# Performance work log

Measured on AMD Instinct MI355X. Metric: run time of the kernel, lower is better.

The kernel has to match this reference:

```python
import jax, jax.numpy as jnp
import numpy as np

# e2m1 nibble -> float LUT (indices 0..7 positive, 8..15 negative), per mxfp4 spec
E2M1_LUT = jnp.array([0.0, 0.5, 1.0, 1.5, 2.0, 3.0, 4.0, 6.0,
                      -0.0, -0.5, -1.0, -1.5, -2.0, -3.0, -4.0, -6.0], dtype=jnp.float32)


def mxfp4_dequant(scales, blocks):
    """scales: [E, R, K//32] int (uint8 values); blocks: [E, R, K//32, 16] int (uint8 values).
    Returns dequantized weight [E, K, R] (transposed like the original)."""
    low = blocks & 15
    high = (blocks >> 4) & 15
    interleaved = jnp.stack([low, high], axis=-1)            # [E, R, K//32, 16, 2]
    interleaved = interleaved.reshape(blocks.shape[:-1] + (32,))  # [E, R, K//32, 32]
    vals = E2M1_LUT[interleaved]                             # [E, R, K//32, 32] f32
    exp = scales.astype(jnp.int32) - 127                     # biased uint8 exponent
    deq = jnp.ldexp(vals, exp[..., None])                    # scale each block
    deq = deq.reshape(deq.shape[:-2] + (-1,))                # [E, R, K]
    return deq.transpose(0, 2, 1)                            # [E, K, R]


def rmsnorm(x, w, eps=1e-5):
    var = jnp.mean(x * x, axis=-1, keepdims=True)
    return x * jax.lax.rsqrt(var + eps) * w


def setup_inputs() -> dict:
    key = jax.random.key(0)
    ks = jax.random.split(key, 8)
    T, H, D, E = 1024, 2048, 2048, 8
    return {
        "x": jax.random.normal(ks[0], (T, H), dtype=jnp.float32),
        "norm_weight": jnp.ones((H,), dtype=jnp.float32),
        "router_weight": jax.random.normal(ks[1], (H, E), dtype=jnp.float32) * 0.02,
        "router_bias": jnp.zeros((E,), dtype=jnp.float32),
        "gate_up_scales": jax.random.randint(ks[2], (E, 2 * D, H // 32), 0, 132, dtype=jnp.int32),
        "gate_up_blocks": jax.random.randint(ks[3], (E, 2 * D, H // 32, 16), 0, 256, dtype=jnp.int32),
        "gate_up_bias": jax.random.normal(ks[4], (E, 2 * D), dtype=jnp.float32) * 0.02,
        "down_scales": jax.random.randint(ks[5], (E, H, D // 32), 0, 132, dtype=jnp.int32),
        "down_blocks": jax.random.randint(ks[6], (E, H, D // 32, 16), 0, 256, dtype=jnp.int32),
        "down_bias": jax.random.normal(ks[7], (E, H), dtype=jnp.float32) * 0.02,
        "k": 4,
    }


def reference(x, norm_weight, router_weight, router_bias,
              gate_up_scales, gate_up_blocks, gate_up_bias,
              down_scales, down_blocks, down_bias, k):
    alpha, limit = 1.702, 7.0
    W_gu = mxfp4_dequant(gate_up_scales, gate_up_blocks)   # [E, H, 2D]
    W_down = mxfp4_dequant(down_scales, down_blocks)       # [E, D, H]

    t = rmsnorm(x, norm_weight)                            # [T, H]
    logits = t @ router_weight + router_bias               # [T, E]
    top_v, top_i = jax.lax.top_k(logits, k)                # [T, k]
    top_v = jax.nn.softmax(top_v, axis=-1)
    tok = jnp.arange(logits.shape[0])[:, None]             # [T, 1]
    scores = jnp.zeros_like(logits).at[tok, top_i].set(top_v)  # [T, E]

    # dense all-expert compute, masked post-hoc by router scores (as in original)
    gate_up = jnp.einsum('th,ehd->etd', t, W_gu) + gate_up_bias[:, None, :]  # [E, T, 2D]
    gate = jnp.minimum(gate_up[..., ::2], limit)
    up = jnp.clip(gate_up[..., 1::2], -limit, limit)
    glu = gate * jax.nn.sigmoid(gate * alpha)
    nxt = jnp.einsum('etd,edh->eth', (up + 1.0) * glu, W_down) + down_bias[:, None, :]  # [E, T, H]
    nxt = nxt * scores.T[..., None]                        # weight by router scores
    return jnp.sum(nxt, axis=0) + x
```

## Files before the change

### kernel.cpp

```cpp
#include <hip/hip_runtime.h>
#include <hip/hip_bf16.h>
#include <stdint.h>

#define T_TOK 1024
#define HDIM 2048
#define DDIM 2048
#define NE 8

typedef unsigned int uint;
typedef unsigned short ushort;

typedef _Float16 f16x8 __attribute__((ext_vector_type(8)));
typedef float f32x4 __attribute__((ext_vector_type(4)));

typedef __attribute__((address_space(1))) const void v_g;
typedef __attribute__((address_space(3))) void v_l;

__device__ __forceinline__ ushort f2h(float f) {
  _Float16 h = (_Float16)f;
  return *(ushort*)&h;
}

__device__ __forceinline__ uint dqh(uint nib, int sc) {
  uint m = nib & 7u;
  int e = (int)(m >> 1);
  int e16 = sc - 113 + e;
  uint mant = ((m & 1u) && m >= 2u) ? 0x200u : 0u;
  uint bits;
  if (m == 0u || e16 <= -10) bits = 0u;
  else if (e16 >= 1) bits = ((uint)e16 << 10) | mant;
  else bits = (0x400u | mant) >> (1 - e16);
  return bits | ((nib & 8u) << 12);
}
__device__ __forceinline__ uint dq2h(uint b, int sc) {
  return dqh(b & 15u, sc) | (dqh((b >> 4) & 15u, sc) << 16);
}

__device__ __forceinline__ void waitv4() {
  asm volatile("s_waitcnt vmcnt(4)" ::: "memory");
  __builtin_amdgcn_sched_barrier(0);
}
__device__ __forceinline__ void waitv0() {
  asm volatile("s_waitcnt vmcnt(0)" ::: "memory");
  __builtin_amdgcn_sched_barrier(0);
}
__device__ __forceinline__ void barrier_raw() {
  asm volatile("" ::: "memory");
  __builtin_amdgcn_s_barrier();
  asm volatile("" ::: "memory");
}

__device__ __forceinline__ void router_body(
    int t, const float* __restrict__ x, const float* __restrict__ nw,
    const float* __restrict__ rw, const float* __restrict__ rb,
    ushort* __restrict__ tbuf, float* __restrict__ scores)
{
  const int tid = threadIdx.x;
  const float4* xr = (const float4*)(x + (size_t)t * HDIM);
  float4 v0 = xr[tid * 2], v1 = xr[tid * 2 + 1];
  float ss = v0.x*v0.x + v0.y*v0.y + v0.z*v0.z + v0.w*v0.w
           + v1.x*v1.x + v1.y*v1.y + v1.z*v1.z + v1.w*v1.w;
  __shared__ float red[256];
  red[tid] = ss;
  __syncthreads();
  for (int s = 128; s > 0; s >>= 1) {
    if (tid < s) red[tid] += red[tid + s];
    __syncthreads();
  }
  const float rstd = rsqrtf(red[0] * (1.0f / HDIM) + 1e-5f);
  float xv[8] = {v0.x, v0.y, v0.z, v0.w, v1.x, v1.y, v1.z, v1.w};
  float lp[NE];
#pragma unroll
  for (int e = 0; e < NE; ++e) lp[e] = 0.f;
  union { ushort us[8]; uint4 v; } pkh;
  const int h0 = tid * 8;
#pragma unroll
  for (int j = 0; j < 8; ++j) {
    int h = h0 + j;
    float tn = xv[j] * rstd * nw[h];
    pkh.us[j] = f2h(tn);
#pragma unroll
    for (int e = 0; e < NE; ++e) lp[e] += tn * rw[h * NE + e];
  }
  *(uint4*)(tbuf + (size_t)t * HDIM + h0) = pkh.v;
#pragma unroll
  for (int e = 0; e < NE; ++e)
#pragma unroll
    for (int off = 32; off > 0; off >>= 1) lp[e] += __shfl_down(lp[e], off);
  __shared__ float wred[4][NE];
  if ((tid & 63) == 0) {
#pragma unroll
    for (int e = 0; e < NE; ++e) wred[tid >> 6][e] = lp[e];
  }
  __syncthreads();
  if (tid == 0) {
    float lg[NE];
#pragma unroll
    for (int e = 0; e < NE; ++e)
      lg[e] = wred[0][e] + wred[1][e] + wred[2][e] + wred[3][e] + rb[e];
    bool used[NE] = {false, false, false, false, false, false, false, false};
    float tv[4]; int ti[4];
    for (int s = 0; s < 4; ++s) {
      float best = -3.4e38f; int bi = 0;
      for (int e = 0; e < NE; ++e)
        if (!used[e] && lg[e] > best) { best = lg[e]; bi = e; }
      used[bi] = true; tv[s] = best; ti[s] = bi;
    }
    float den = 0.f, ev[4];
    for (int s = 0; s < 4; ++s) { ev[s] = expf(tv[s] - tv[0]); den += ev[s]; }
    float so[NE] = {0, 0, 0, 0, 0, 0, 0, 0};
    for (int s = 0; s < 4; ++s) so[ti[s]] = ev[s] / den;
#pragma unroll
    for (int e = 0; e < NE; ++e) scores[t * NE + e] = so[e];
  }
}

__global__ __launch_bounds__(256) void router_kernel(
    const float* __restrict__ x, const float* __restrict__ nw,
    const float* __restrict__ rw, const float* __restrict__ rb,
    ushort* __restrict__ tbuf, float* __restrict__ scores)
{
  router_body(blockIdx.x, x, nw, rw, rb, tbuf, scores);
}

#define NDQB ((NE * 4096 * 64 + NE * 2048 * 64) / 256)
__global__ __launch_bounds__(256) void prep_kernel(
    const float* __restrict__ x, const float* __restrict__ nw,
    const float* __restrict__ rw, const float* __restrict__ rb,
    const int* __restrict__ gub, const int* __restrict__ gus,
    const int* __restrict__ dnb, const int* __restrict__ dns,
    ushort* __restrict__ tbuf, float* __restrict__ scores,
    ushort* __restrict__ wgu, ushort* __restrict__ wdn)
{
  if (blockIdx.x >= NDQB) {
    router_body(blockIdx.x - NDQB, x, nw, rw, rb, tbuf, scores);
    return;
  }
  const int NG = NE * 4096 * 64;
  int tidg = blockIdx.x * 256 + threadIdx.x;
  const int* qb; const int* qs; ushort* dst; int bi;
  if (tidg < NG) { bi = tidg; qb = gub; qs = gus; dst = wgu; }
  else           { bi = tidg - NG; qb = dnb; qs = dns; dst = wdn; }
  int sc = qs[bi];
  const int4* bp = (const int4*)(qb + (size_t)bi * 16);
  int4 q0 = bp[0], q1 = bp[1], q2 = bp[2], q3 = bp[3];
  uint w[16];
  w[0]=dq2h(q0.x,sc);  w[1]=dq2h(q0.y,sc);  w[2]=dq2h(q0.z,sc);  w[3]=dq2h(q0.w,sc);
  w[4]=dq2h(q1.x,sc);  w[5]=dq2h(q1.y,sc);  w[6]=dq2h(q1.z,sc);  w[7]=dq2h(q1.w,sc);
  w[8]=dq2h(q2.x,sc);  w[9]=dq2h(q2.y,sc);  w[10]=dq2h(q2.z,sc); w[11]=dq2h(q2.w,sc);
  w[12]=dq2h(q3.x,sc); w[13]=dq2h(q3.y,sc); w[14]=dq2h(q3.z,sc); w[15]=dq2h(q3.w,sc);
  uint4* o = (uint4*)(dst + (size_t)bi * 32);
  o[0] = make_uint4(w[0], w[1], w[2], w[3]);
  o[1] = make_uint4(w[4], w[5], w[6], w[7]);
  o[2] = make_uint4(w[8], w[9], w[10], w[11]);
  o[3] = make_uint4(w[12], w[13], w[14], w[15]);
}

__global__ __launch_bounds__(256) void scan_kernel(
    const float* __restrict__ scores, int* __restrict__ cnts, int* __restrict__ idx)
{
  const int e = blockIdx.x, tid = threadIdx.x;
  int loc[4], c = 0;
#pragma unroll
  for (int j = 0; j < 4; ++j) {
    int t = tid * 4 + j;
    loc[j] = (scores[t * NE + e] != 0.f) ? 1 : 0;
    c += loc[j];
  }
  __shared__ int sc[256];
  sc[tid] = c;
  __syncthreads();
  for (int off = 1; off < 256; off <<= 1) {
    int v = (tid >= off) ? sc[tid - off] : 0;
    __syncthreads();
    sc[tid] += v;
    __syncthreads();
  }
  int base = sc[tid] - c;
#pragma unroll
  for (int j = 0; j < 4; ++j)
    if (loc[j]) idx[e * T_TOK + base++] = tid * 4 + j;
  if (tid == 255) cnts[e] = sc[255];
}

template<int MODE>
__global__ __launch_bounds__(256) void mx_gemm_p(
    const ushort* __restrict__ Abase,
    const ushort* __restrict__ Bw,
    const float* __restrict__ bias,
    const float* __restrict__ scores,
    const int* __restrict__ cnts,
    const int* __restrict__ tokidx,
    ushort* __restrict__ midH,
    float* __restrict__ outp)
{
  constexpr int NTOT = (MODE == 0) ? 2 * DDIM : HDIM;
  constexpr int K    = (MODE == 0) ? HDIM : DDIM;
  constexpr int NKT  = K / 32;
  const int nt = blockIdx.x, mt = blockIdx.y, e = blockIdx.z;
  const int cnt = cnts[e];
  const int m0 = mt * 128, n0 = nt * 128;
  if (m0 >= cnt) return;
  const ushort* A = Abase + (MODE == 0 ? (size_t)0 : (size_t)e * T_TOK * DDIM);

  __shared__ __align__(16) ushort As[2][128 * 32];
  __shared__ __align__(16) ushort Bs[2][128 * 32];
  __shared__ int tok_s[128];

  const int tid = threadIdx.x;
  const int lane = tid & 63;
  const int wv = tid >> 6;
  const int wm = wv >> 1, wn = wv & 1;
  const int fr = lane & 15, kg = lane >> 4;

  if (tid < 128) {
    int sl = m0 + tid;
    tok_s[tid] = (sl < cnt) ? tokidx[e * T_TOK + sl] : 0;
  }
  __syncthreads();

  int arow[2];
#pragma unroll
  for (int j = 0; j < 2; ++j) {
    int row = (tid + 256 * j) >> 2;
    arow[j] = (MODE == 0) ? tok_s[row] : (m0 + row);
  }

  f32x4 acc[4][4];
#pragma unroll
  for (int i = 0; i < 4; ++i)
#pragma unroll
    for (int j = 0; j < 4; ++j) acc[i][j] = f32x4{0.f, 0.f, 0.f, 0.f};

  auto do_stage = [&](int buf, int kt) {
#pragma unroll
    for (int j = 0; j < 2; ++j) {
      int cidx = tid + 256 * j;
      int row = cidx >> 2, ck = cidx & 3;
      int gck = ck ^ ((row >> 1) & 3);
      size_t go = (size_t)arow[j] * K + kt * 32 + gck * 8;
      __builtin_amdgcn_global_load_lds((v_g*)(A + go),
          (v_l*)((char*)&As[buf][0] + cidx * 16), 16, 0, 0);
    }
#pragma unroll
    for (int j = 0; j < 2; ++j) {
      int cidx = tid + 256 * j;
      int row = cidx >> 2, ck = cidx & 3;
      int gck = ck ^ ((row >> 1) & 3);
      const ushort* g = Bw + ((size_t)e * NTOT + n0 + row) * K + kt * 32 + gck * 8;
      __builtin_amdgcn_global_load_lds((v_g*)g,
          (v_l*)((char*)&Bs[buf][0] + cidx * 16), 16, 0, 0);
    }
  };

  auto do_compute = [&](int buf) {
    f16x8 aF[4], bF[4];
#pragma unroll
    for (int mi = 0; mi < 4; ++mi) {
      int r = wm * 64 + mi * 16 + fr;
      int ck = kg ^ ((r >> 1) & 3);
      aF[mi] = *(const f16x8*)(&As[buf][r * 32 + ck * 8]);
    }
#pragma unroll
    for (int ni = 0; ni < 4; ++ni) {
      int r = wn * 64 + ni * 16 + fr;
      int ck = kg ^ ((r >> 1) & 3);
      bF[ni] = *(const f16x8*)(&Bs[buf][r * 32 + ck * 8]);
    }
#pragma unroll
    for (int mi = 0; mi < 4; ++mi)
#pragma unroll
      for (int ni = 0; ni < 4; ++ni)
        acc[mi][ni] = __builtin_amdgcn_mfma_f32_16x16x32_f16(aF[mi], bF[ni], acc[mi][ni], 0, 0, 0);
  };

  do_stage(0, 0);
  do_stage(1, 1);
  waitv4();
  barrier_raw();
#pragma unroll 2
  for (int kt = 0; kt < NKT; ++kt) {
    do_compute(kt & 1);
    if (kt == NKT - 1) break;
    barrier_raw();
    if (kt + 2 < NKT) {
      do_stage(kt & 1, kt + 2);
      waitv4();
    } else {
      waitv0();
    }
    barrier_raw();
  }

  const int c = lane & 15, rg = lane >> 4;
  const int sbase = m0 + wm * 64, nbase = n0 + wn * 64;
  if constexpr (MODE == 0) {
#pragma unroll
    for (int mi = 0; mi < 4; ++mi)
#pragma unroll
      for (int ni = 0; ni < 4; ++ni) {
        int n = nbase + ni * 16 + c;
        float bv = bias[(size_t)e * NTOT + n];
#pragma unroll
        for (int r = 0; r < 4; ++r) {
          int slot = sbase + mi * 16 + rg * 4 + r;
          float val = acc[mi][ni][r] + bv;
          float other = __shfl_xor(val, 1);
          if (!(c & 1) && slot < cnt) {
            int tok = tok_s[slot - m0];
            float g = fminf(val, 7.0f);
            float u = fminf(fmaxf(other, -7.0f), 7.0f);
            float glu = g / (1.0f + expf(-1.702f * g));
            float mv = (u + 1.0f) * glu;
            float s = scores[tok * NE + e];
            midH[((size_t)e * T_TOK + slot) * DDIM + ((uint)n >> 1)] = f2h(mv * s);
          }
        }
      }
  } else {
#pragma unroll
    for (int mi = 0; mi < 4; ++mi)
#pragma unroll
      for (int ni = 0; ni < 4; ++ni) {
        int n = nbase + ni * 16 + c;
        float dbv = bias[(size_t)e * NTOT + n];
#pragma unroll
        for (int r = 0; r < 4; ++r) {
          int slot = sbase + mi * 16 + rg * 4 + r;
          if (slot < cnt) {
            int tok = tok_s[slot - m0];
            float s = scores[tok * NE + e];
            atomicAdd(outp + (size_t)tok * HDIM + n, acc[mi][ni][r] + s * dbv);
          }
        }
      }
  }
}

__global__ __launch_bounds__(256) void gu_gemm_q(
    const ushort* __restrict__ At,
    const int* __restrict__ qblocks,
    const int* __restrict__ qscales,
    const float* __restrict__ bias,
    const float* __restrict__ scores,
    const int* __restrict__ cnts,
    const int* __restrict__ tokidx,
    ushort* __restrict__ midH)
{
  constexpr int NTOT = 2 * DDIM;
  constexpr int K = HDIM;
  const int nt = blockIdx.x, mt = blockIdx.y, e = blockIdx.z;
  const int cnt = cnts[e];
  const int m0 = mt * 128, n0 = nt * 128;
  if (m0 >= cnt) return;

  __shared__ __align__(16) ushort As[128 * 64];
  __shared__ __align__(16) ushort Bs[128 * 64];
  __shared__ int tok_s[128];

  const int tid = threadIdx.x;
  const int lane = tid & 63;
  const int wv = tid >> 6;
  const int wm = wv >> 1, wn = wv & 1;
  const int fr = lane & 15, kg = lane >> 4;

  if (tid < 128) {
    int sl = m0 + tid;
    tok_s[tid] = (sl < cnt) ? tokidx[e * T_TOK + sl] : 0;
  }
  __syncthreads();
  int arow[4];
#pragma unroll
  for (int j = 0; j < 4; ++j) arow[j] = tok_s[(tid + 256 * j) >> 3];

  f32x4 acc[4][4];
#pragma unroll
  for (int i = 0; i < 4; ++i)
#pragma unroll
    for (int j = 0; j < 4; ++j) acc[i][j] = f32x4{0.f, 0.f, 0.f, 0.f};

  for (int kt = 0; kt < K / 64; ++kt) {
#pragma unroll
    for (int j = 0; j < 4; ++j) {
      int cidx = tid + 256 * j;
      int row = cidx >> 3, ck = cidx & 7;
      int sck = ck ^ (row & 7);
      size_t go = (size_t)arow[j] * K + kt * 64 + sck * 8;
      __builtin_amdgcn_global_load_lds((v_g*)(At + go), (v_l*)((char*)As + cidx * 16), 16, 0, 0);
    }
    {
      const int brow = tid >> 1, bblk = tid & 1;
      int kb = kt * 2 + bblk;
      size_t bi = ((size_t)e * NTOT + n0 + brow) * (K / 32) + kb;
      int sc = qscales[bi];
      const int4* bp = (const int4*)(qblocks + bi * 16);
      int4 q0 = bp[0], q1 = bp[1], q2 = bp[2], q3 = bp[3];
      uint w[16];
      w[0]=dq2h(q0.x,sc);  w[1]=dq2h(q0.y,sc);  w[2]=dq2h(q0.z,sc);  w[3]=dq2h(q0.w,sc);
      w[4]=dq2h(q1.x,sc);  w[5]=dq2h(q1.y,sc);  w[6]=dq2h(q1.z,sc);  w[7]=dq2h(q1.w,sc);
      w[8]=dq2h(q2.x,sc);  w[9]=dq2h(q2.y,sc);  w[10]=dq2h(q2.z,sc); w[11]=dq2h(q2.w,sc);
      w[12]=dq2h(q3.x,sc); w[13]=dq2h(q3.y,sc); w[14]=dq2h(q3.z,sc); w[15]=dq2h(q3.w,sc);
#pragma unroll
      for (int q = 0; q < 4; ++q) {
        int ck = bblk * 4 + q;
        int sk = ck ^ (brow & 7);
        *(uint4*)((char*)Bs + brow * 128 + sk * 16) =
            make_uint4(w[4*q], w[4*q+1], w[4*q+2], w[4*q+3]);
      }
    }
    __syncthreads();
#pragma unroll
    for (int kh = 0; kh < 2; ++kh) {
      f16x8 aF[4], bF[4];
#pragma unroll
      for (int mi = 0; mi < 4; ++mi) {
        int r = wm * 64 + mi * 16 + fr;
        int ck = (kh * 4 + kg) ^ (r & 7);
        aF[mi] = *(const f16x8*)((const char*)As + r * 128 + ck * 16);
      }
#pragma unroll
      for (int ni = 0; ni < 4; ++ni) {
        int r = wn * 64 + ni * 16 + fr;
        int ck = (kh * 4 + kg) ^ (r & 7);
        bF[ni] = *(const f16x8*)((const char*)Bs + r * 128 + ck * 16);
      }
#pragma unroll
      for (int mi = 0; mi < 4; ++mi)
#pragma unroll
        for (int ni = 0; ni < 4; ++ni)
          acc[mi][ni] = __builtin_amdgcn_mfma_f32_16x16x32_f16(aF[mi], bF[ni], acc[mi][ni], 0, 0, 0);
    }
    __syncthreads();
  }

  const int c = lane & 15, rg = lane >> 4;
  const int sbase = m0 + wm * 64, nbase = n0 + wn * 64;
#pragma unroll
  for (int mi = 0; mi < 4; ++mi)
#pragma unroll
    for (int ni = 0; ni < 4; ++ni) {
      int n = nbase + ni * 16 + c;
      float bv = bias[(size_t)e * NTOT + n];
#pragma unroll
      for (int r = 0; r < 4; ++r) {
        int slot = sbase + mi * 16 + rg * 4 + r;
        float val = acc[mi][ni][r] + bv;
        float other = __shfl_xor(val, 1);
        if (!(c & 1) && slot < cnt) {
          int tok = tok_s[slot - m0];
          float g = fminf(val, 7.0f);
          float u = fminf(fmaxf(other, -7.0f), 7.0f);
          float glu = g / (1.0f + expf(-1.702f * g));
          float mv = (u + 1.0f) * glu;
          float s = scores[tok * NE + e];
          midH[((size_t)e * T_TOK + slot) * DDIM + ((uint)n >> 1)] = f2h(mv * s);
        }
      }
    }
}

__global__ __launch_bounds__(256) void dn_gemm_q(
    const ushort* __restrict__ Abase,
    const int* __restrict__ qblocks,
    const int* __restrict__ qscales,
    const float* __restrict__ bias,
    const float* __restrict__ scores,
    const int* __restrict__ cnts,
    const int* __restrict__ tokidx,
    float* __restrict__ outp)
{
  constexpr int NTOT = HDIM;
  constexpr int K    = DDIM;
  const int nt = blockIdx.x, mt = blockIdx.y, e = blockIdx.z;
  const int cnt = cnts[e];
  const int m0 = mt * 128, n0 = nt * 128;
  if (m0 >= cnt) return;
  const ushort* A = Abase + (size_t)e * T_TOK * DDIM;

  __shared__ __align__(16) ushort As[128 * 64];
  __shared__ __align__(16) ushort Bs[128 * 64];
  __shared__ int tok_s[128];

  const int tid = threadIdx.x;
  const int lane = tid & 63;
  const int wv = tid >> 6;
  const int wm = wv >> 1, wn = wv & 1;
  const int fr = lane & 15, kg = lane >> 4;

  if (tid < 128) {
    int sl = m0 + tid;
    tok_s[tid] = (sl < cnt) ? tokidx[e * T_TOK + sl] : 0;
  }
  __syncthreads();

  f32x4 acc[4][4];
#pragma unroll
  for (int i = 0; i < 4; ++i)
#pragma unroll
    for (int j = 0; j < 4; ++j) acc[i][j] = f32x4{0.f, 0.f, 0.f, 0.f};

  for (int kt = 0; kt < K / 64; ++kt) {
#pragma unroll
    for (int j = 0; j < 4; ++j) {
      int cidx = tid + 256 * j;
      int row = cidx >> 3, ck = cidx & 7;
      int sck = ck ^ (row & 7);
      size_t go = (size_t)(m0 + row) * K + kt * 64 + sck * 8;
      __builtin_amdgcn_global_load_lds((v_g*)(A + go), (v_l*)((char*)As + cidx * 16), 16, 0, 0);
    }
    {
      const int brow = tid >> 1, bblk = tid & 1;
      int kb = kt * 2 + bblk;
      size_t bi = ((size_t)e * NTOT + n0 + brow) * (K / 32) + kb;
      int sc = qscales[bi];
      const int4* bp = (const int4*)(qblocks + bi * 16);
      int4 q0 = bp[0], q1 = bp[1], q2 = bp[2], q3 = bp[3];
      uint w[16];
      w[0]=dq2h(q0.x,sc);  w[1]=dq2h(q0.y,sc);  w[2]=dq2h(q0.z,sc);  w[3]=dq2h(q0.w,sc);
      w[4]=dq2h(q1.x,sc);  w[5]=dq2h(q1.y,sc);  w[6]=dq2h(q1.z,sc);  w[7]=dq2h(q1.w,sc);
      w[8]=dq2h(q2.x,sc);  w[9]=dq2h(q2.y,sc);  w[10]=dq2h(q2.z,sc); w[11]=dq2h(q2.w,sc);
      w[12]=dq2h(q3.x,sc); w[13]=dq2h(q3.y,sc); w[14]=dq2h(q3.z,sc); w[15]=dq2h(q3.w,sc);
#pragma unroll
      for (int q = 0; q < 4; ++q) {
        int ck = bblk * 4 + q;
        int sk = ck ^ (brow & 7);
        *(uint4*)((char*)Bs + brow * 128 + sk * 16) =
            make_uint4(w[4*q], w[4*q+1], w[4*q+2], w[4*q+3]);
      }
    }
    __syncthreads();
#pragma unroll
    for (int kh = 0; kh < 2; ++kh) {
      f16x8 aF[4], bF[4];
#pragma unroll
      for (int mi = 0; mi < 4; ++mi) {
        int r = wm * 64 + mi * 16 + fr;
        int ck = (kh * 4 + kg) ^ (r & 7);
        aF[mi] = *(const f16x8*)((const char*)As + r * 128 + ck * 16);
      }
#pragma unroll
      for (int ni = 0; ni < 4; ++ni) {
        int r = wn * 64 + ni * 16 + fr;
        int ck = (kh * 4 + kg) ^ (r & 7);
        bF[ni] = *(const f16x8*)((const char*)Bs + r * 128 + ck * 16);
      }
#pragma unroll
      for (int mi = 0; mi < 4; ++mi)
#pragma unroll
        for (int ni = 0; ni < 4; ++ni)
          acc[mi][ni] = __builtin_amdgcn_mfma_f32_16x16x32_f16(aF[mi], bF[ni], acc[mi][ni], 0, 0, 0);
    }
    __syncthreads();
  }

  const int c = lane & 15, rg = lane >> 4;
  const int sbase = m0 + wm * 64, nbase = n0 + wn * 64;
#pragma unroll
  for (int mi = 0; mi < 4; ++mi)
#pragma unroll
    for (int ni = 0; ni < 4; ++ni) {
      int n = nbase + ni * 16 + c;
      float dbv = bias[(size_t)e * NTOT + n];
#pragma unroll
      for (int r = 0; r < 4; ++r) {
        int slot = sbase + mi * 16 + rg * 4 + r;
        if (slot < cnt) {
          int tok = tok_s[slot - m0];
          float s = scores[tok * NE + e];
          atomicAdd(outp + (size_t)tok * HDIM + n, acc[mi][ni][r] + s * dbv);
        }
      }
    }
}

extern "C" void kernel_launch(void* const* d_in, const int* in_sizes, int n_in,
                              void* d_out, int out_size, void* d_ws, size_t ws_size,
                              hipStream_t stream)
{
  const float* x      = (const float*)d_in[0];
  const float* nw     = (const float*)d_in[1];
  const float* rw     = (const float*)d_in[2];
  const float* rb     = (const float*)d_in[3];
  const int*   gus    = (const int*)d_in[4];
  const int*   gub    = (const int*)d_in[5];
  const float* gubias = (const float*)d_in[6];
  const int*   dns    = (const int*)d_in[7];
  const int*   dnb    = (const int*)d_in[8];
  const float* dnbias = (const float*)d_in[9];

  char* ws = (char*)d_ws;
  const size_t SZ_WGU = (size_t)NE * 4096 * 2048 * 2;
  const size_t SZ_WDN = (size_t)NE * 2048 * 2048 * 2;
  const size_t SZ_T   = (size_t)T_TOK * HDIM * 2;
  const size_t SZ_MID = (size_t)NE * T_TOK * DDIM * 2;
  const size_t SZ_SC  = (size_t)T_TOK * NE * 4;
  const size_t SZ_IDX = (size_t)NE * T_TOK * 4;
  const size_t SZ_CNT = 128;

  const size_t need_act = SZ_T + SZ_MID + SZ_SC + SZ_IDX + SZ_CNT;
  const bool predeq = ws_size >= SZ_WGU + SZ_WDN + need_act;
  ushort* wgu = (ushort*)ws;
  ushort* wdn = (ushort*)(ws + SZ_WGU);
  char* base2 = predeq ? (ws + SZ_WGU + SZ_WDN) : ws;
  ushort* tbuf   = (ushort*)base2;
  ushort* midHp  = (ushort*)(base2 + SZ_T);
  float*  scores = (float*)(base2 + SZ_T + SZ_MID);
  int*    cnts   = (int*)(base2 + SZ_T + SZ_MID + SZ_SC);
  int*    tokidx = (int*)(base2 + SZ_T + SZ_MID + SZ_SC + SZ_CNT);
  float*  outp   = (float*)d_out;

  hipMemcpyAsync(d_out, (void*)x, (size_t)T_TOK * HDIM * 4, hipMemcpyDeviceToDevice, stream);
  if (predeq) {
    prep_kernel<<<NDQB + T_TOK, 256, 0, stream>>>(
        x, nw, rw, rb, gub, gus, dnb, dns, tbuf, scores, wgu, wdn);
    scan_kernel<<<NE, 256, 0, stream>>>(scores, cnts, tokidx);
    mx_gemm_p<0><<<dim3(32, 8, NE), 256, 0, stream>>>(
        tbuf, wgu, gubias, scores, cnts, tokidx, midHp, nullptr);
    mx_gemm_p<1><<<dim3(16, 8, NE), 256, 0, stream>>>(
        midHp, wdn, dnbias, scores, cnts, tokidx, nullptr, outp);
  } else {
    router_kernel<<<T_TOK, 256, 0, stream>>>(x, nw, rw, rb, tbuf, scores);
    scan_kernel<<<NE, 256, 0, stream>>>(scores, cnts, tokidx);
    gu_gemm_q<<<dim3(32, 8, NE), 256, 0, stream>>>(
        tbuf, gub, gus, gubias, scores, cnts, tokidx, midHp);
    dn_gemm_q<<<dim3(16, 8, NE), 256, 0, stream>>>(
        midHp, dnb, dns, dnbias, scores, cnts, tokidx, outp);
  }
}
```

Measured before the change: 344.2 us.

## Replace down-GEMM atomic scatter with per-expert stores and a token gather

Adds a third down-projection GEMM mode that writes each expert's per-slot result to a dense fp32 buffer with plain stores instead of atomically adding into the output. A slot map from the scan kernel tells a new gather kernel where each token's rows sit, and that kernel sums the expert contributions with the residual x and the scaled down bias. This also removes the separate device-to-device copy of x into the output. The aim is to avoid atomic contention and read-modify-write traffic on the output, at the cost of an extra 64 MB workspace buffer, its write and read-back, and one more kernel launch. The new path runs only when the workspace is large enough.

New measurement: 318.1 us. 7.6% less time.

```diff
diff --git a/kernel.cpp b/kernel.cpp
--- a/kernel.cpp
+++ b/kernel.cpp
@@ -157,7 +157,8 @@
 }
 
 __global__ __launch_bounds__(256) void scan_kernel(
-    const float* __restrict__ scores, int* __restrict__ cnts, int* __restrict__ idx)
+    const float* __restrict__ scores, int* __restrict__ cnts,
+    int* __restrict__ idx, int* __restrict__ slotmap)
 {
   const int e = blockIdx.x, tid = threadIdx.x;
   int loc[4], c = 0;
@@ -179,7 +180,12 @@
   int base = sc[tid] - c;
 #pragma unroll
   for (int j = 0; j < 4; ++j)
-    if (loc[j]) idx[e * T_TOK + base++] = tid * 4 + j;
+    if (loc[j]) {
+      int t = tid * 4 + j;
+      idx[e * T_TOK + base] = t;
+      slotmap[t * NE + e] = base;
+      base++;
+    }
   if (tid == 255) cnts[e] = sc[255];
 }
 
@@ -317,7 +323,7 @@
           }
         }
       }
-  } else {
+  } else if constexpr (MODE == 1) {
 #pragma unroll
     for (int mi = 0; mi < 4; ++mi)
 #pragma unroll
@@ -334,7 +340,53 @@
           }
         }
       }
-  }
+  } else {
+#pragma unroll
+    for (int mi = 0; mi < 4; ++mi)
+#pragma unroll
+      for (int ni = 0; ni < 4; ++ni) {
+        int n = nbase + ni * 16 + c;
+#pragma unroll
+        for (int r = 0; r < 4; ++r) {
+          int slot = sbase + mi * 16 + rg * 4 + r;
+          if (slot < cnt)
+            outp[((size_t)e * T_TOK + slot) * HDIM + n] = acc[mi][ni][r];
+        }
+      }
+  }
+}
+
+__global__ __launch_bounds__(256) void gather_kernel(
+    const float* __restrict__ x, const float* __restrict__ midD,
+    const float* __restrict__ dnbias, const float* __restrict__ scores,
+    const int* __restrict__ slotmap, float* __restrict__ outp)
+{
+  const int t = blockIdx.x, tid = threadIdx.x;
+  const int h0 = tid * 8;
+  const float4* xr = (const float4*)(x + (size_t)t * HDIM + h0);
+  float4 a0 = xr[0], a1 = xr[1];
+  float sc[NE]; int sl[NE];
+#pragma unroll
+  for (int e = 0; e < NE; ++e) sc[e] = scores[t * NE + e];
+#pragma unroll
+  for (int e = 0; e < NE; ++e) sl[e] = slotmap[t * NE + e];
+#pragma unroll
+  for (int e = 0; e < NE; ++e) {
+    if (sc[e] != 0.f) {
+      const float4* mr = (const float4*)(midD + ((size_t)e * T_TOK + sl[e]) * HDIM + h0);
+      const float4* br = (const float4*)(dnbias + (size_t)e * HDIM + h0);
+      float4 m0 = mr[0], m1 = mr[1];
+      float4 b0 = br[0], b1 = br[1];
+      float s = sc[e];
+      a0.x += m0.x + s * b0.x; a0.y += m0.y + s * b0.y;
+      a0.z += m0.z + s * b0.z; a0.w += m0.w + s * b0.w;
+      a1.x += m1.x + s * b1.x; a1.y += m1.y + s * b1.y;
+      a1.z += m1.z + s * b1.z; a1.w += m1.w + s * b1.w;
+    }
+  }
+  float4* orow = (float4*)(outp + (size_t)t * HDIM + h0);
+  orow[0] = a0;
+  orow[1] = a1;
 }
 
 __global__ __launch_bounds__(256) void gu_gemm_q(
@@ -589,16 +641,21 @@
   const float* dnbias = (const float*)d_in[9];
 
   char* ws = (char*)d_ws;
-  const size_t SZ_WGU = (size_t)NE * 4096 * 2048 * 2;
-  const size_t SZ_WDN = (size_t)NE * 2048 * 2048 * 2;
-  const size_t SZ_T   = (size_t)T_TOK * HDIM * 2;
-  const size_t SZ_MID = (size_t)NE * T_TOK * DDIM * 2;
-  const size_t SZ_SC  = (size_t)T_TOK * NE * 4;
-  const size_t SZ_IDX = (size_t)NE * T_TOK * 4;
-  const size_t SZ_CNT = 128;
-
-  const size_t need_act = SZ_T + SZ_MID + SZ_SC + SZ_IDX + SZ_CNT;
-  const bool predeq = ws_size >= SZ_WGU + SZ_WDN + need_act;
+  const size_t SZ_WGU  = (size_t)NE * 4096 * 2048 * 2;
+  const size_t SZ_WDN  = (size_t)NE * 2048 * 2048 * 2;
+  const size_t SZ_T    = (size_t)T_TOK * HDIM * 2;
+  const size_t SZ_MID  = (size_t)NE * T_TOK * DDIM * 2;
+  const size_t SZ_MIDD = (size_t)NE * T_TOK * HDIM * 4;
+  const size_t SZ_SC   = (size_t)T_TOK * NE * 4;
+  const size_t SZ_IDX  = (size_t)NE * T_TOK * 4;
+  const size_t SZ_SLOT = (size_t)T_TOK * NE * 4;
+  const size_t SZ_CNT  = 128;
+
+  const size_t need_mid = SZ_WGU + SZ_WDN + SZ_T + SZ_MID + SZ_SC + SZ_IDX + SZ_SLOT + SZ_CNT;
+  const size_t need_big = need_mid + SZ_MIDD;
+  const bool predeq = ws_size >= need_mid;
+  const bool bigws  = ws_size >= need_big;
+
   ushort* wgu = (ushort*)ws;
   ushort* wdn = (ushort*)(ws + SZ_WGU);
   char* base2 = predeq ? (ws + SZ_WGU + SZ_WDN) : ws;
@@ -607,20 +664,32 @@
   float*  scores = (float*)(base2 + SZ_T + SZ_MID);
   int*    cnts   = (int*)(base2 + SZ_T + SZ_MID + SZ_SC);
   int*    tokidx = (int*)(base2 + SZ_T + SZ_MID + SZ_SC + SZ_CNT);
+  int*    slotmap= (int*)(base2 + SZ_T + SZ_MID + SZ_SC + SZ_CNT + SZ_IDX);
+  float*  midD   = (float*)(base2 + SZ_T + SZ_MID + SZ_SC + SZ_CNT + SZ_IDX + SZ_SLOT);
   float*  outp   = (float*)d_out;
 
-  hipMemcpyAsync(d_out, (void*)x, (size_t)T_TOK * HDIM * 4, hipMemcpyDeviceToDevice, stream);
   if (predeq) {
     prep_kernel<<<NDQB + T_TOK, 256, 0, stream>>>(
         x, nw, rw, rb, gub, gus, dnb, dns, tbuf, scores, wgu, wdn);
-    scan_kernel<<<NE, 256, 0, stream>>>(scores, cnts, tokidx);
+    scan_kernel<<<NE, 256, 0, stream>>>(scores, cnts, tokidx, slotmap);
     mx_gemm_p<0><<<dim3(32, 8, NE), 256, 0, stream>>>(
         tbuf, wgu, gubias, scores, cnts, tokidx, midHp, nullptr);
-    mx_gemm_p<1><<<dim3(16, 8, NE), 256, 0, stream>>>(
-        midHp, wdn, dnbias, scores, cnts, tokidx, nullptr, outp);
+    if (bigws) {
+      mx_gemm_p<2><<<dim3(16, 8, NE), 256, 0, stream>>>(
+          midHp, wdn, dnbias, scores, cnts, tokidx, nullptr, midD);
+      gather_kernel<<<T_TOK, 256, 0, stream>>>(
+          x, midD, dnbias, scores, slotmap, outp);
+    } else {
+      hipMemcpyAsync(d_out, (void*)x, (size_t)T_TOK * HDIM * 4,
+                     hipMemcpyDeviceToDevice, stream);
+      mx_gemm_p<1><<<dim3(16, 8, NE), 256, 0, stream>>>(
+          midHp, wdn, dnbias, scores, cnts, tokidx, nullptr, outp);
+    }
   } else {
+    hipMemcpyAsync(d_out, (void*)x, (size_t)T_TOK * HDIM * 4,
+                   hipMemcpyDeviceToDevice, stream);
     router_kernel<<<T_TOK, 256, 0, stream>>>(x, nw, rw, rb, tbuf, scores);
-    scan_kernel<<<NE, 256, 0, stream>>>(scores, cnts, tokidx);
+    scan_kernel<<<NE, 256, 0, stream>>>(scores, cnts, tokidx, slotmap);
     gu_gemm_q<<<dim3(32, 8, NE), 256, 0, stream>>>(
         tbuf, gub, gus, gubias, scores, cnts, tokidx, midHp);
     dn_gemm_q<<<dim3(16, 8, NE), 256, 0, stream>>>(
```
